# Kernel tuning notes

Measured on AMD Instinct MI355X. Metric: run time of the kernel, lower is better.

The kernel has to match this reference:

```python
import jax, jax.numpy as jnp
import numpy as np

B, T, TC, C, CC, H = 2, 2048, 512, 1024, 512, 16
D = C // H  # head dim = 64


def setup_inputs() -> dict:
    key = jax.random.key(0)
    ks = jax.random.split(key, 18)
    w = lambda k, i, o: (jax.random.normal(k, (i, o), jnp.float32) / np.sqrt(i).astype(np.float32))
    return {
        "x": jax.random.normal(ks[0], (B, T, C), jnp.float32),
        "cross_input": jax.random.normal(ks[1], (B, TC, CC), jnp.float32),
        "Wk": w(ks[2], C, C),  "bk": jnp.zeros((C,), jnp.float32),
        "Wq": w(ks[3], C, C),  "bq": jnp.zeros((C,), jnp.float32),
        "Wv": w(ks[4], C, C),  "bv": jnp.zeros((C,), jnp.float32),
        "Wck": w(ks[5], CC, C), "bck": jnp.zeros((C,), jnp.float32),
        "Wcq": w(ks[6], C, C),  "bcq": jnp.zeros((C,), jnp.float32),
        "Wcv": w(ks[7], CC, C), "bcv": jnp.zeros((C,), jnp.float32),
        "Wp": w(ks[8], C, C),   "bp": jnp.zeros((C,), jnp.float32),
    }


def _heads(t):
    # [B, L, C] -> [B, H, L, D]
    b, l, _ = t.shape
    return t.reshape(b, l, H, D).transpose(0, 2, 1, 3)


def reference(x, cross_input, Wk, bk, Wq, bq, Wv, bv, Wck, bck, Wcq, bcq, Wcv, bcv, Wp, bp):
    scale = np.float32(1.0 / np.sqrt(D))
    q = _heads(x @ Wq + bq)
    k = _heads(x @ Wk + bk)
    v = _heads(x @ Wv + bv)
    # causal self-attention with materialized scores (faithful to original)
    att = jnp.einsum("bhqd,bhkd->bhqk", q, k) * scale
    causal = jnp.tril(jnp.ones((T, T), bool))
    att = jnp.where(causal[None, None], att, -jnp.inf)
    y = jnp.einsum("bhqk,bhkd->bhqd", jax.nn.softmax(att, axis=-1), v)
    # cross-attention (no mask)
    qc = _heads(x @ Wcq + bcq)
    kc = _heads(cross_input @ Wck + bck)
    vc = _heads(cross_input @ Wcv + bcv)
    attc = jnp.einsum("bhqd,bhkd->bhqk", qc, kc) * scale
    y = y + jnp.einsum("bhqk,bhkd->bhqd", jax.nn.softmax(attc, axis=-1), vc)
    # merge heads + output projection (dropout prob = 0 -> identity)
    y = y.transpose(0, 2, 1, 3).reshape(x.shape[0], T, C)
    return y @ Wp + bp
```

## Files before the change

### kernel.cpp

```cpp
#include <hip/hip_runtime.h>
#include <hip/hip_bf16.h>
#include <type_traits>

typedef __bf16 bf16;
typedef __bf16 bf16x8 __attribute__((ext_vector_type(8)));
typedef float floatx4 __attribute__((ext_vector_type(4)));
typedef unsigned int uint32x4 __attribute__((ext_vector_type(4)));

#if __has_builtin(__builtin_amdgcn_exp2f)
#define EXP2(x) __builtin_amdgcn_exp2f(x)
#else
#define EXP2(x) exp2f(x)
#endif

__device__ __forceinline__ void glds16(const bf16* g, bf16* l) {
  __builtin_amdgcn_global_load_lds((const __attribute__((address_space(1))) void*)g,
                                   (__attribute__((address_space(3))) void*)l, 16, 0, 0);
}

__device__ __forceinline__ unsigned pack_bf16(float a, float b) {
  unsigned short ua = __builtin_bit_cast(unsigned short, (bf16)a);
  unsigned short ub = __builtin_bit_cast(unsigned short, (bf16)b);
  return (unsigned)ua | ((unsigned)ub << 16);
}

struct PrepArgs {
  const float* x; const float* xc;
  bf16* xbf; bf16* xcbf;
  const float* b4[4];
  const float* bc[2];
  float* bias4; float* biasc;
  const float* W[7];
  bf16* WT[7];
};

__global__ __launch_bounds__(256) void prep_kernel(PrepArgs a) {
  __shared__ bf16 tsh[32][33];
  const int bx = blockIdx.x, tid = threadIdx.x;
  if (bx < 4096) {
    int i = bx * 256 + tid;
    float4 f = ((const float4*)a.x)[i];
    bf16 t[4] = {(bf16)f.x, (bf16)f.y, (bf16)f.z, (bf16)f.w};
    *(uint2*)&a.xbf[(long)i * 4] = *(const uint2*)t;
  } else if (bx < 4608) {
    int i = (bx - 4096) * 256 + tid;
    float4 f = ((const float4*)a.xc)[i];
    bf16 t[4] = {(bf16)f.x, (bf16)f.y, (bf16)f.z, (bf16)f.w};
    *(uint2*)&a.xcbf[(long)i * 4] = *(const uint2*)t;
  } else if (bx < 4632) {
    int lb = bx - 4608;
    if (lb < 16) {
      int i = lb * 256 + tid;
      int sec = i >> 10;
      float v = a.b4[sec][i & 1023];
      if (sec == 0 || sec == 3) v *= 0.18033688f;
      a.bias4[i] = v;
    } else {
      int i = (lb - 16) * 256 + tid;
      a.biasc[i] = a.bc[i >> 10][i & 1023];
    }
  } else {
    int t = bx - 4632, w, R, bxw, byw;
    if (t < 5120) { w = t >> 10; R = 1024; int l = t & 1023; bxw = l & 31; byw = l >> 5; }
    else { int t2 = t - 5120; w = 5 + (t2 >> 9); R = 512; int l = t2 & 511; bxw = l & 31; byw = l >> 5; }
    const float* in = a.W[w];
    bf16* out = a.WT[w];
    const float sc = (w == 0 || w == 3) ? 0.18033688f : 1.0f;
    int tx = tid & 31, ty = tid >> 5;
    int c = bxw * 32 + tx;
#pragma unroll
    for (int i = 0; i < 4; i++) {
      int r = byw * 32 + ty + i * 8;
      tsh[ty + i * 8][tx] = (bf16)(in[(long)r * 1024 + c] * sc);
    }
    __syncthreads();
    int oc = byw * 32 + tx;
#pragma unroll
    for (int i = 0; i < 4; i++) {
      int orr = bxw * 32 + ty + i * 8;
      out[(long)orr * R + oc] = tsh[tx][ty + i * 8];
    }
  }
}

template <typename OutT>
__global__ __launch_bounds__(256, 4) void gemm128(const bf16* __restrict__ A,
                                                  const bf16* __restrict__ Bt,
                                                  const float* __restrict__ bias,
                                                  OutT* __restrict__ C,
                                                  int M, int N, int K, int ldc,
                                                  bf16* __restrict__ Vt,
                                                  int vcol0, int vcol1, int Lt, int tok_shift) {
  __shared__ alignas(16) bf16 As[128 * 32];
  __shared__ alignas(16) bf16 Bs[128 * 32];
  const int tid = threadIdx.x, wave = tid >> 6, lane = tid & 63;
  const int l16 = lane & 15, l4 = lane >> 4;
  const int wm = wave & 1, wn = wave >> 1;
  const int nwg = gridDim.x * gridDim.y;
  int lin = blockIdx.y * gridDim.x + blockIdx.x;
  lin = (lin & 7) * (nwg >> 3) + (lin >> 3);
  const int n0 = (lin % gridDim.x) * 128, m0 = (lin / gridDim.x) * 128;
  const int lrow = lane >> 2, lch = (lane & 3) * 8;

  floatx4 acc[4][4];
#pragma unroll
  for (int mt = 0; mt < 4; mt++)
#pragma unroll
    for (int nt = 0; nt < 4; nt++) acc[mt][nt] = (floatx4){0.f, 0.f, 0.f, 0.f};

  const bf16* Ag = A + (long)(m0 + wave * 32 + lrow) * K + lch;
  const bf16* Bg = Bt + (long)(n0 + wave * 32 + lrow) * K + lch;
  bf16* Al = &As[(wave * 32) * 32];
  bf16* Bl = &Bs[(wave * 32) * 32];

  for (int k0 = 0; k0 < K; k0 += 32) {
    __syncthreads();
    glds16(Ag + k0, Al);
    glds16(Ag + k0 + (long)16 * K, Al + 16 * 32);
    glds16(Bg + k0, Bl);
    glds16(Bg + k0 + (long)16 * K, Bl + 16 * 32);
    __syncthreads();
    bf16x8 a[4], b[4];
#pragma unroll
    for (int mt = 0; mt < 4; mt++) a[mt] = *(const bf16x8*)&As[(wm * 64 + mt * 16 + l16) * 32 + l4 * 8];
#pragma unroll
    for (int nt = 0; nt < 4; nt++) b[nt] = *(const bf16x8*)&Bs[(wn * 64 + nt * 16 + l16) * 32 + l4 * 8];
#pragma unroll
    for (int mt = 0; mt < 4; mt++)
#pragma unroll
      for (int nt = 0; nt < 4; nt++)
        acc[mt][nt] = __builtin_amdgcn_mfma_f32_16x16x32_bf16(a[mt], b[nt], acc[mt][nt], 0, 0, 0);
  }

  const bool vpath = (vcol0 >= 0) && (n0 >= vcol0) && (n0 < vcol1);
  if (!vpath) {
    const int coladj = (vcol0 >= 0 && n0 >= vcol1) ? (vcol1 - vcol0) : 0;
#pragma unroll
    for (int nt = 0; nt < 4; nt++) {
      int col = n0 + wn * 64 + nt * 16 + l16;
      float bv = bias[col];
#pragma unroll
      for (int mt = 0; mt < 4; mt++)
#pragma unroll
        for (int r = 0; r < 4; r++) {
          int row = m0 + wm * 64 + mt * 16 + l4 * 4 + r;
          float v = acc[mt][nt][r] + bv;
          if constexpr (std::is_same_v<OutT, float>) C[(long)row * ldc + col - coladj] = v;
          else                                       C[(long)row * ldc + col - coladj] = (bf16)v;
        }
    }
  } else {
#pragma unroll
    for (int nt = 0; nt < 4; nt++) {
      int col = n0 + wn * 64 + nt * 16 + l16;
      int c = col - vcol0, hh = c >> 6, dd = c & 63;
      float bv = bias[col];
#pragma unroll
      for (int mt = 0; mt < 4; mt++) {
        int t0 = m0 + wm * 64 + mt * 16 + l4 * 4;
        int bb = t0 >> tok_shift, t = t0 & ((1 << tok_shift) - 1);
        t = (t & ~31) | (((t >> 2) & 3) << 3) | (((t >> 4) & 1) << 2) | (t & 3);
        bf16 tmp[4];
#pragma unroll
        for (int r = 0; r < 4; r++) tmp[r] = (bf16)(acc[mt][nt][r] + bv);
        *(uint2*)&Vt[(((long)bb * 16 + hh) * 64 + dd) * Lt + t] = *(const uint2*)tmp;
      }
    }
  }
}

__global__ __launch_bounds__(256, 2) void attn_kernel(const bf16* __restrict__ QKQc,
                                                      const bf16* __restrict__ VtB,
                                                      const bf16* __restrict__ KcB,
                                                      const bf16* __restrict__ VctB,
                                                      bf16* __restrict__ Y) {
  __shared__ float Lbuf[4][4][16];
  __shared__ alignas(16) bf16 U2[4 * 64 * 40];
  __shared__ alignas(16) float Osave[256][20];
  __shared__ alignas(16) bf16 Vsl[4][2][2048];
  const int tid = threadIdx.x, w = tid >> 6, lane = tid & 63;
  const int l16 = lane & 15, l4 = lane >> 4;
  const int bh = blockIdx.x, h = bh & 15, b = bh >> 4;
  const int wk = w * 32;
  const float NEG = -1e30f;
  const int swv = (l4 ^ ((l16 >> 1) & 3)) * 8;

  for (int qi = 0; qi < 2; qi++) {
    const int qt = qi ? (int)blockIdx.y : 31 - (int)blockIdx.y;
    const int q0 = qt * 64;

    for (int phase = 0; phase < 2; phase++) {
      const bf16 *Qb, *Kb, *Vtb;
      int kstr, vtstr, nkt;
      if (phase == 0) {
        Qb = QKQc + (long)b * 2048 * 3072 + h * 64;
        Kb = Qb + 1024;                              kstr = 3072;
        Vtb = VtB + ((long)b * 16 + h) * 64 * 2048;  vtstr = 2048;
        nkt = (qt + 2) >> 1;
      } else {
        Qb = QKQc + (long)b * 2048 * 3072 + h * 64 + 2048;
        Kb = KcB + (long)b * 512 * 1024 + h * 64;    kstr = 1024;
        Vtb = VctB + ((long)b * 16 + h) * 64 * 512;  vtstr = 512;
        nkt = 4;
      }

      __syncthreads();

      bf16x8 qf[4][2];
#pragma unroll
      for (int qtt = 0; qtt < 4; qtt++) {
        const bf16* qp = Qb + (long)(q0 + qtt * 16 + l16) * 3072 + l4 * 8;
#pragma unroll
        for (int ds = 0; ds < 2; ds++) qf[qtt][ds] = *(const bf16x8*)(qp + ds * 32);
      }

      float l_i[4];
#pragma unroll
      for (int qtt = 0; qtt < 4; qtt++) l_i[qtt] = 0.f;
      floatx4 oacc[4][4];
#pragma unroll
      for (int mtd = 0; mtd < 4; mtd++)
#pragma unroll
        for (int qtt = 0; qtt < 4; qtt++) oacc[mtd][qtt] = (floatx4){0.f, 0.f, 0.f, 0.f};

      bf16x8 kreg[2][2];
#pragma unroll
      for (int mt = 0; mt < 2; mt++)
#pragma unroll
        for (int ds = 0; ds < 2; ds++)
          kreg[mt][ds] = *(const bf16x8*)(Kb + (long)(wk + mt * 16 + l16) * kstr + ds * 32 + l4 * 8);
#pragma unroll
      for (int i = 0; i < 4; i++) {
        int c = i * 64 + lane, r = c >> 2;
        int kc = ((c & 3) ^ ((r >> 1) & 3)) * 8;
        glds16(Vtb + (long)r * vtstr + wk + kc, &Vsl[w][0][i * 512]);
      }

      floatx4 sacc[2][4];
#pragma unroll
      for (int mt = 0; mt < 2; mt++)
#pragma unroll
        for (int qtt = 0; qtt < 4; qtt++) sacc[mt][qtt] = (floatx4){0.f, 0.f, 0.f, 0.f};
#pragma unroll
      for (int ds = 0; ds < 2; ds++)
#pragma unroll
        for (int mt = 0; mt < 2; mt++)
#pragma unroll
          for (int qtt = 0; qtt < 4; qtt++)
            sacc[mt][qtt] = __builtin_amdgcn_mfma_f32_16x16x32_bf16(kreg[mt][ds], qf[qtt][ds], sacc[mt][qtt], 0, 0, 0);

      for (int kt = 0; kt < nkt; kt++) {
        const int kbase = kt * 128 + wk;
        const bool more = (kt + 1 < nkt);

        if (more) {
          bf16* dst = &Vsl[w][(kt + 1) & 1][0];
          const int nb = kbase + 128;
#pragma unroll
          for (int i = 0; i < 4; i++) {
            int c = i * 64 + lane, r = c >> 2;
            int kc = ((c & 3) ^ ((r >> 1) & 3)) * 8;
            glds16(Vtb + (long)r * vtstr + nb + kc, dst + i * 512);
          }
        }

        if (phase == 0 && kt == nkt - 1) {
#pragma unroll
          for (int mt = 0; mt < 2; mt++) {
            int keyb = kbase + mt * 16 + l4 * 4;
#pragma unroll
            for (int qtt = 0; qtt < 4; qtt++) {
              int q = q0 + qtt * 16 + l16;
#pragma unroll
              for (int r = 0; r < 4; r++)
                if (keyb + r > q) sacc[mt][qtt][r] = NEG;
            }
          }
        }

        bf16x8 vc[4];
        {
          const bf16* sl = &Vsl[w][kt & 1][0];
          if (more) asm volatile("s_waitcnt vmcnt(4)" ::: "memory");
          else      asm volatile("s_waitcnt vmcnt(0)" ::: "memory");
#pragma unroll
          for (int mtd = 0; mtd < 4; mtd++)
            vc[mtd] = *(const bf16x8*)&sl[(mtd * 16 + l16) * 32 + swv];
        }

        if (more) {
          const int nb = kbase + 128;
#pragma unroll
          for (int mt = 0; mt < 2; mt++)
#pragma unroll
            for (int ds = 0; ds < 2; ds++)
              kreg[mt][ds] = *(const bf16x8*)(Kb + (long)(nb + mt * 16 + l16) * kstr + ds * 32 + l4 * 8);
        }

#pragma unroll
        for (int qtt = 0; qtt < 4; qtt++) {
          float p0 = EXP2(sacc[0][qtt][0]), p1 = EXP2(sacc[0][qtt][1]);
          float p2 = EXP2(sacc[0][qtt][2]), p3 = EXP2(sacc[0][qtt][3]);
          float p4 = EXP2(sacc[1][qtt][0]), p5 = EXP2(sacc[1][qtt][1]);
          float p6 = EXP2(sacc[1][qtt][2]), p7 = EXP2(sacc[1][qtt][3]);
          l_i[qtt] += ((p0 + p1) + (p2 + p3)) + ((p4 + p5) + (p6 + p7));
          uint32x4 pu = {pack_bf16(p0, p1), pack_bf16(p2, p3), pack_bf16(p4, p5), pack_bf16(p6, p7)};
          bf16x8 pf = __builtin_bit_cast(bf16x8, pu);
          __builtin_amdgcn_s_setprio(1);
#pragma unroll
          for (int mtd = 0; mtd < 4; mtd++)
            oacc[mtd][qtt] = __builtin_amdgcn_mfma_f32_16x16x32_bf16(vc[mtd], pf, oacc[mtd][qtt], 0, 0, 0);
          __builtin_amdgcn_s_setprio(0);
        }

        if (more) {
#pragma unroll
          for (int mt = 0; mt < 2; mt++)
#pragma unroll
            for (int qtt = 0; qtt < 4; qtt++) sacc[mt][qtt] = (floatx4){0.f, 0.f, 0.f, 0.f};
          __builtin_amdgcn_s_setprio(1);
#pragma unroll
          for (int ds = 0; ds < 2; ds++)
#pragma unroll
            for (int mt = 0; mt < 2; mt++)
#pragma unroll
              for (int qtt = 0; qtt < 4; qtt++)
                sacc[mt][qtt] = __builtin_amdgcn_mfma_f32_16x16x32_bf16(kreg[mt][ds], qf[qtt][ds], sacc[mt][qtt], 0, 0, 0);
          __builtin_amdgcn_s_setprio(0);
        }
      }

      float lsum[4];
#pragma unroll
      for (int qtt = 0; qtt < 4; qtt++) {
        float r = l_i[qtt];
        r += __shfl_xor(r, 16);
        r += __shfl_xor(r, 32);
        lsum[qtt] = r;
      }
      if (l4 == 0) {
#pragma unroll
        for (int qtt = 0; qtt < 4; qtt++) Lbuf[w][qtt][l16] = lsum[qtt];
      }
      float sum[16];
#pragma unroll
      for (int j = 0; j < 16; j++) sum[j] = 0.f;
      float denom = 0.f;
#pragma unroll
      for (int p = 0; p < 2; p++) {
        __syncthreads();
#pragma unroll
        for (int qtt = 0; qtt < 4; qtt++)
#pragma unroll
          for (int mm = 0; mm < 2; mm++) {
            int mtd = p * 2 + mm;
            uint2 u = {pack_bf16(oacc[mtd][qtt][0], oacc[mtd][qtt][1]),
                       pack_bf16(oacc[mtd][qtt][2], oacc[mtd][qtt][3])};
            *(uint2*)&U2[((w * 64) + qtt * 16 + l16) * 40 + mm * 16 + l4 * 4] = u;
          }
        __syncthreads();
        if (p == 0)
          denom = Lbuf[0][w][l16] + Lbuf[1][w][l16] + Lbuf[2][w][l16] + Lbuf[3][w][l16];
        if ((l4 >> 1) == p) {
#pragma unroll
          for (int s = 0; s < 4; s++) {
            bf16x8 c0 = *(const bf16x8*)&U2[((s * 64) + w * 16 + l16) * 40 + (l4 & 1) * 16];
            bf16x8 c1 = *(const bf16x8*)&U2[((s * 64) + w * 16 + l16) * 40 + (l4 & 1) * 16 + 8];
#pragma unroll
            for (int j = 0; j < 8; j++) { sum[j] += (float)c0[j]; sum[8 + j] += (float)c1[j]; }
          }
        }
      }
      float invd = 1.0f / denom;
      if (phase == 0) {
#pragma unroll
        for (int jj = 0; jj < 4; jj++) {
          float4 v = {sum[jj * 4] * invd, sum[jj * 4 + 1] * invd,
                      sum[jj * 4 + 2] * invd, sum[jj * 4 + 3] * invd};
          *(float4*)&Osave[tid][jj * 4] = v;
        }
      } else {
        long row = (long)b * 2048 + q0 + w * 16 + l16;
        bf16 out[16];
#pragma unroll
        for (int jj = 0; jj < 4; jj++) {
          float4 v = *(const float4*)&Osave[tid][jj * 4];
          out[jj * 4]     = (bf16)(v.x + sum[jj * 4] * invd);
          out[jj * 4 + 1] = (bf16)(v.y + sum[jj * 4 + 1] * invd);
          out[jj * 4 + 2] = (bf16)(v.z + sum[jj * 4 + 2] * invd);
          out[jj * 4 + 3] = (bf16)(v.w + sum[jj * 4 + 3] * invd);
        }
        *(bf16x8*)&Y[row * 1024 + h * 64 + l4 * 16] = *(const bf16x8*)&out[0];
        *(bf16x8*)&Y[row * 1024 + h * 64 + l4 * 16 + 8] = *(const bf16x8*)&out[8];
      }
    }
  }
}

extern "C" void kernel_launch(void* const* d_in, const int* in_sizes, int n_in,
                              void* d_out, int out_size, void* d_ws, size_t ws_size,
                              hipStream_t stream) {
  const float* x   = (const float*)d_in[0];
  const float* xc  = (const float*)d_in[1];
  const float* Wk  = (const float*)d_in[2];  const float* bk  = (const float*)d_in[3];
  const float* Wq  = (const float*)d_in[4];  const float* bq  = (const float*)d_in[5];
  const float* Wv  = (const float*)d_in[6];  const float* bv  = (const float*)d_in[7];
  const float* Wck = (const float*)d_in[8];  const float* bck = (const float*)d_in[9];
  const float* Wcq = (const float*)d_in[10]; const float* bcq = (const float*)d_in[11];
  const float* Wcv = (const float*)d_in[12]; const float* bcv = (const float*)d_in[13];
  const float* Wp  = (const float*)d_in[14]; const float* bp  = (const float*)d_in[15];

  char* ws = (char*)d_ws;
  const size_t MB = 1ull << 20;
  bf16*  WT_all = (bf16*)(ws + 0);
  bf16*  WC_all = (bf16*)(ws + 8 * MB);
  bf16*  WpT    = (bf16*)(ws + 10 * MB);
  bf16*  xbf    = (bf16*)(ws + 12 * MB);
  bf16*  Yb     = xbf;
  bf16*  xcbf   = (bf16*)(ws + 20 * MB);
  float* bias4  = (float*)(ws + 21 * MB);
  float* biasc  = (float*)(ws + 21 * MB + 65536);
  bf16*  QKQc   = (bf16*)(ws + 22 * MB);
  bf16*  VtB    = (bf16*)(ws + 46 * MB);
  bf16*  KcB    = (bf16*)(ws + 54 * MB);
  bf16*  VctB   = (bf16*)(ws + 56 * MB);

  PrepArgs pa;
  pa.x = x; pa.xc = xc; pa.xbf = xbf; pa.xcbf = xcbf;
  pa.b4[0] = bq; pa.b4[1] = bk; pa.b4[2] = bv; pa.b4[3] = bcq;
  pa.bc[0] = bck; pa.bc[1] = bcv;
  pa.bias4 = bias4; pa.biasc = biasc;
  pa.W[0] = Wq;  pa.WT[0] = WT_all + 0ll * 1024 * 1024;
  pa.W[1] = Wk;  pa.WT[1] = WT_all + 1ll * 1024 * 1024;
  pa.W[2] = Wv;  pa.WT[2] = WT_all + 2ll * 1024 * 1024;
  pa.W[3] = Wcq; pa.WT[3] = WT_all + 3ll * 1024 * 1024;
  pa.W[4] = Wp;  pa.WT[4] = WpT;
  pa.W[5] = Wck; pa.WT[5] = WC_all + 0ll * 1024 * 512;
  pa.W[6] = Wcv; pa.WT[6] = WC_all + 1ll * 1024 * 512;
  prep_kernel<<<10776, 256, 0, stream>>>(pa);

  gemm128<bf16><<<dim3(32, 32), 256, 0, stream>>>(xbf, WT_all, bias4, QKQc,
                                                  4096, 4096, 1024, 3072,
                                                  VtB, 2048, 3072, 2048, 11);
  gemm128<bf16><<<dim3(16, 8), 256, 0, stream>>>(xcbf, WC_all, biasc, KcB,
                                                 1024, 2048, 512, 1024,
                                                 VctB, 1024, 2048, 512, 9);

  attn_kernel<<<dim3(32, 16), 256, 0, stream>>>(QKQc, VtB, KcB, VctB, Yb);

  gemm128<float><<<dim3(8, 32), 256, 0, stream>>>(Yb, WpT, bp, (float*)d_out,
                                                  4096, 1024, 1024, 1024,
                                                  nullptr, -1, -1, 0, 0);
}
```

Measured before the change: 245.8 us.

## Give each attention block one query tile and shrink LDS footprint

Result: no change. 243.1 us (-1.1%).

```diff
diff --git a/kernel.cpp b/kernel.cpp
--- a/kernel.cpp
+++ b/kernel.cpp
@@ -176,223 +176,214 @@
                                                       bf16* __restrict__ Y) {
   __shared__ float Lbuf[4][4][16];
   __shared__ alignas(16) bf16 U2[4 * 64 * 40];
-  __shared__ alignas(16) float Osave[256][20];
-  __shared__ alignas(16) bf16 Vsl[4][2][2048];
+  __shared__ alignas(16) bf16 Osave[256][24];
+  __shared__ alignas(16) bf16 Vsl[4][2048];
   const int tid = threadIdx.x, w = tid >> 6, lane = tid & 63;
   const int l16 = lane & 15, l4 = lane >> 4;
   const int bh = blockIdx.x, h = bh & 15, b = bh >> 4;
+  const int qt = 31 - (int)blockIdx.y;
+  const int q0 = qt * 64;
   const int wk = w * 32;
   const float NEG = -1e30f;
   const int swv = (l4 ^ ((l16 >> 1) & 3)) * 8;
 
-  for (int qi = 0; qi < 2; qi++) {
-    const int qt = qi ? (int)blockIdx.y : 31 - (int)blockIdx.y;
-    const int q0 = qt * 64;
-
-    for (int phase = 0; phase < 2; phase++) {
-      const bf16 *Qb, *Kb, *Vtb;
-      int kstr, vtstr, nkt;
-      if (phase == 0) {
-        Qb = QKQc + (long)b * 2048 * 3072 + h * 64;
-        Kb = Qb + 1024;                              kstr = 3072;
-        Vtb = VtB + ((long)b * 16 + h) * 64 * 2048;  vtstr = 2048;
-        nkt = (qt + 2) >> 1;
-      } else {
-        Qb = QKQc + (long)b * 2048 * 3072 + h * 64 + 2048;
-        Kb = KcB + (long)b * 512 * 1024 + h * 64;    kstr = 1024;
-        Vtb = VctB + ((long)b * 16 + h) * 64 * 512;  vtstr = 512;
-        nkt = 4;
-      }
-
-      __syncthreads();
-
-      bf16x8 qf[4][2];
-#pragma unroll
-      for (int qtt = 0; qtt < 4; qtt++) {
-        const bf16* qp = Qb + (long)(q0 + qtt * 16 + l16) * 3072 + l4 * 8;
-#pragma unroll
-        for (int ds = 0; ds < 2; ds++) qf[qtt][ds] = *(const bf16x8*)(qp + ds * 32);
-      }
-
-      float l_i[4];
-#pragma unroll
-      for (int qtt = 0; qtt < 4; qtt++) l_i[qtt] = 0.f;
-      floatx4 oacc[4][4];
-#pragma unroll
-      for (int mtd = 0; mtd < 4; mtd++)
-#pragma unroll
-        for (int qtt = 0; qtt < 4; qtt++) oacc[mtd][qtt] = (floatx4){0.f, 0.f, 0.f, 0.f};
-
-      bf16x8 kreg[2][2];
+  for (int phase = 0; phase < 2; phase++) {
+    const bf16 *Qb, *Kb, *Vtb;
+    int kstr, vtstr, nkt;
+    if (phase == 0) {
+      Qb = QKQc + (long)b * 2048 * 3072 + h * 64;
+      Kb = Qb + 1024;                              kstr = 3072;
+      Vtb = VtB + ((long)b * 16 + h) * 64 * 2048;  vtstr = 2048;
+      nkt = (qt + 2) >> 1;
+    } else {
+      Qb = QKQc + (long)b * 2048 * 3072 + h * 64 + 2048;
+      Kb = KcB + (long)b * 512 * 1024 + h * 64;    kstr = 1024;
+      Vtb = VctB + ((long)b * 16 + h) * 64 * 512;  vtstr = 512;
+      nkt = 4;
+    }
+
+    __syncthreads();
+
+    bf16x8 qf[4][2];
+#pragma unroll
+    for (int qtt = 0; qtt < 4; qtt++) {
+      const bf16* qp = Qb + (long)(q0 + qtt * 16 + l16) * 3072 + l4 * 8;
+#pragma unroll
+      for (int ds = 0; ds < 2; ds++) qf[qtt][ds] = *(const bf16x8*)(qp + ds * 32);
+    }
+
+    float l_i[4];
+#pragma unroll
+    for (int qtt = 0; qtt < 4; qtt++) l_i[qtt] = 0.f;
+    floatx4 oacc[4][4];
+#pragma unroll
+    for (int mtd = 0; mtd < 4; mtd++)
+#pragma unroll
+      for (int qtt = 0; qtt < 4; qtt++) oacc[mtd][qtt] = (floatx4){0.f, 0.f, 0.f, 0.f};
+
+    bf16x8 kreg[2][2];
+#pragma unroll
+    for (int mt = 0; mt < 2; mt++)
+#pragma unroll
+      for (int ds = 0; ds < 2; ds++)
+        kreg[mt][ds] = *(const bf16x8*)(Kb + (long)(wk + mt * 16 + l16) * kstr + ds * 32 + l4 * 8);
+#pragma unroll
+    for (int i = 0; i < 4; i++) {
+      int c = i * 64 + lane, r = c >> 2;
+      int kc = ((c & 3) ^ ((r >> 1) & 3)) * 8;
+      glds16(Vtb + (long)r * vtstr + wk + kc, &Vsl[w][i * 512]);
+    }
+
+    floatx4 sacc[2][4];
+#pragma unroll
+    for (int mt = 0; mt < 2; mt++)
+#pragma unroll
+      for (int qtt = 0; qtt < 4; qtt++) sacc[mt][qtt] = (floatx4){0.f, 0.f, 0.f, 0.f};
+#pragma unroll
+    for (int ds = 0; ds < 2; ds++)
 #pragma unroll
       for (int mt = 0; mt < 2; mt++)
 #pragma unroll
-        for (int ds = 0; ds < 2; ds++)
-          kreg[mt][ds] = *(const bf16x8*)(Kb + (long)(wk + mt * 16 + l16) * kstr + ds * 32 + l4 * 8);
-#pragma unroll
-      for (int i = 0; i < 4; i++) {
-        int c = i * 64 + lane, r = c >> 2;
-        int kc = ((c & 3) ^ ((r >> 1) & 3)) * 8;
-        glds16(Vtb + (long)r * vtstr + wk + kc, &Vsl[w][0][i * 512]);
-      }
-
-      floatx4 sacc[2][4];
-#pragma unroll
-      for (int mt = 0; mt < 2; mt++)
-#pragma unroll
-        for (int qtt = 0; qtt < 4; qtt++) sacc[mt][qtt] = (floatx4){0.f, 0.f, 0.f, 0.f};
-#pragma unroll
-      for (int ds = 0; ds < 2; ds++)
-#pragma unroll
-        for (int mt = 0; mt < 2; mt++)
-#pragma unroll
-          for (int qtt = 0; qtt < 4; qtt++)
-            sacc[mt][qtt] = __builtin_amdgcn_mfma_f32_16x16x32_bf16(kreg[mt][ds], qf[qtt][ds], sacc[mt][qtt], 0, 0, 0);
-
-      for (int kt = 0; kt < nkt; kt++) {
-        const int kbase = kt * 128 + wk;
-        const bool more = (kt + 1 < nkt);
-
-        if (more) {
-          bf16* dst = &Vsl[w][(kt + 1) & 1][0];
-          const int nb = kbase + 128;
-#pragma unroll
-          for (int i = 0; i < 4; i++) {
-            int c = i * 64 + lane, r = c >> 2;
-            int kc = ((c & 3) ^ ((r >> 1) & 3)) * 8;
-            glds16(Vtb + (long)r * vtstr + nb + kc, dst + i * 512);
+        for (int qtt = 0; qtt < 4; qtt++)
+          sacc[mt][qtt] = __builtin_amdgcn_mfma_f32_16x16x32_bf16(kreg[mt][ds], qf[qtt][ds], sacc[mt][qtt], 0, 0, 0);
+
+    for (int kt = 0; kt < nkt; kt++) {
+      const int kbase = kt * 128 + wk;
+      const bool more = (kt + 1 < nkt);
+
+      if (phase == 0 && kt == nkt - 1) {
+#pragma unroll
+        for (int mt = 0; mt < 2; mt++) {
+          int keyb = kbase + mt * 16 + l4 * 4;
+#pragma unroll
+          for (int qtt = 0; qtt < 4; qtt++) {
+            int q = q0 + qtt * 16 + l16;
+#pragma unroll
+            for (int r = 0; r < 4; r++)
+              if (keyb + r > q) sacc[mt][qtt][r] = NEG;
           }
         }
-
-        if (phase == 0 && kt == nkt - 1) {
-#pragma unroll
-          for (int mt = 0; mt < 2; mt++) {
-            int keyb = kbase + mt * 16 + l4 * 4;
-#pragma unroll
-            for (int qtt = 0; qtt < 4; qtt++) {
-              int q = q0 + qtt * 16 + l16;
-#pragma unroll
-              for (int r = 0; r < 4; r++)
-                if (keyb + r > q) sacc[mt][qtt][r] = NEG;
-            }
-          }
+      }
+
+      asm volatile("s_waitcnt vmcnt(0)" ::: "memory");
+      bf16x8 vc[4];
+      {
+        const bf16* sl = &Vsl[w][0];
+#pragma unroll
+        for (int mtd = 0; mtd < 4; mtd++)
+          vc[mtd] = *(const bf16x8*)&sl[(mtd * 16 + l16) * 32 + swv];
+      }
+      asm volatile("s_waitcnt lgkmcnt(0)" ::: "memory");
+
+      if (more) {
+        const int nb = kbase + 128;
+#pragma unroll
+        for (int mt = 0; mt < 2; mt++)
+#pragma unroll
+          for (int ds = 0; ds < 2; ds++)
+            kreg[mt][ds] = *(const bf16x8*)(Kb + (long)(nb + mt * 16 + l16) * kstr + ds * 32 + l4 * 8);
+        bf16* dst = &Vsl[w][0];
+#pragma unroll
+        for (int i = 0; i < 4; i++) {
+          int c = i * 64 + lane, r = c >> 2;
+          int kc = ((c & 3) ^ ((r >> 1) & 3)) * 8;
+          glds16(Vtb + (long)r * vtstr + nb + kc, dst + i * 512);
         }
-
-        bf16x8 vc[4];
-        {
-          const bf16* sl = &Vsl[w][kt & 1][0];
-          if (more) asm volatile("s_waitcnt vmcnt(4)" ::: "memory");
-          else      asm volatile("s_waitcnt vmcnt(0)" ::: "memory");
-#pragma unroll
-          for (int mtd = 0; mtd < 4; mtd++)
-            vc[mtd] = *(const bf16x8*)&sl[(mtd * 16 + l16) * 32 + swv];
+      }
+
+#pragma unroll
+      for (int qtt = 0; qtt < 4; qtt++) {
+        float p0 = EXP2(sacc[0][qtt][0]), p1 = EXP2(sacc[0][qtt][1]);
+        float p2 = EXP2(sacc[0][qtt][2]), p3 = EXP2(sacc[0][qtt][3]);
+        float p4 = EXP2(sacc[1][qtt][0]), p5 = EXP2(sacc[1][qtt][1]);
+        float p6 = EXP2(sacc[1][qtt][2]), p7 = EXP2(sacc[1][qtt][3]);
+        l_i[qtt] += ((p0 + p1) + (p2 + p3)) + ((p4 + p5) + (p6 + p7));
+        uint32x4 pu = {pack_bf16(p0, p1), pack_bf16(p2, p3), pack_bf16(p4, p5), pack_bf16(p6, p7)};
+        bf16x8 pf = __builtin_bit_cast(bf16x8, pu);
+        __builtin_amdgcn_s_setprio(1);
+#pragma unroll
+        for (int mtd = 0; mtd < 4; mtd++)
+          oacc[mtd][qtt] = __builtin_amdgcn_mfma_f32_16x16x32_bf16(vc[mtd], pf, oacc[mtd][qtt], 0, 0, 0);
+        __builtin_amdgcn_s_setprio(0);
+      }
+
+      if (more) {
+#pragma unroll
+        for (int mt = 0; mt < 2; mt++)
+#pragma unroll
+          for (int qtt = 0; qtt < 4; qtt++) sacc[mt][qtt] = (floatx4){0.f, 0.f, 0.f, 0.f};
+        __builtin_amdgcn_s_setprio(1);
+#pragma unroll
+        for (int ds = 0; ds < 2; ds++)
+#pragma unroll
+          for (int mt = 0; mt < 2; mt++)
+#pragma unroll
+            for (int qtt = 0; qtt < 4; qtt++)
+              sacc[mt][qtt] = __builtin_amdgcn_mfma_f32_16x16x32_bf16(kreg[mt][ds], qf[qtt][ds], sacc[mt][qtt], 0, 0, 0);
+        __builtin_amdgcn_s_setprio(0);
+      }
+    }
+
+    float lsum[4];
+#pragma unroll
+    for (int qtt = 0; qtt < 4; qtt++) {
+      float r = l_i[qtt];
+      r += __shfl_xor(r, 16);
+      r += __shfl_xor(r, 32);
+      lsum[qtt] = r;
+    }
+    if (l4 == 0) {
+#pragma unroll
+      for (int qtt = 0; qtt < 4; qtt++) Lbuf[w][qtt][l16] = lsum[qtt];
+    }
+    float sum[16];
+#pragma unroll
+    for (int j = 0; j < 16; j++) sum[j] = 0.f;
+    float denom = 0.f;
+#pragma unroll
+    for (int p = 0; p < 2; p++) {
+      __syncthreads();
+#pragma unroll
+      for (int qtt = 0; qtt < 4; qtt++)
+#pragma unroll
+        for (int mm = 0; mm < 2; mm++) {
+          int mtd = p * 2 + mm;
+          uint2 u = {pack_bf16(oacc[mtd][qtt][0], oacc[mtd][qtt][1]),
+                     pack_bf16(oacc[mtd][qtt][2], oacc[mtd][qtt][3])};
+          *(uint2*)&U2[((w * 64) + qtt * 16 + l16) * 40 + mm * 16 + l4 * 4] = u;
         }
-
-        if (more) {
-          const int nb = kbase + 128;
-#pragma unroll
-          for (int mt = 0; mt < 2; mt++)
-#pragma unroll
-            for (int ds = 0; ds < 2; ds++)
-              kreg[mt][ds] = *(const bf16x8*)(Kb + (long)(nb + mt * 16 + l16) * kstr + ds * 32 + l4 * 8);
+      __syncthreads();
+      if (p == 0)
+        denom = Lbuf[0][w][l16] + Lbuf[1][w][l16] + Lbuf[2][w][l16] + Lbuf[3][w][l16];
+      if ((l4 >> 1) == p) {
+#pragma unroll
+        for (int s = 0; s < 4; s++) {
+          bf16x8 c0 = *(const bf16x8*)&U2[((s * 64) + w * 16 + l16) * 40 + (l4 & 1) * 16];
+          bf16x8 c1 = *(const bf16x8*)&U2[((s * 64) + w * 16 + l16) * 40 + (l4 & 1) * 16 + 8];
+#pragma unroll
+          for (int j = 0; j < 8; j++) { sum[j] += (float)c0[j]; sum[8 + j] += (float)c1[j]; }
         }
-
-#pragma unroll
-        for (int qtt = 0; qtt < 4; qtt++) {
-          float p0 = EXP2(sacc[0][qtt][0]), p1 = EXP2(sacc[0][qtt][1]);
-          float p2 = EXP2(sacc[0][qtt][2]), p3 = EXP2(sacc[0][qtt][3]);
-          float p4 = EXP2(sacc[1][qtt][0]), p5 = EXP2(sacc[1][qtt][1]);
-          float p6 = EXP2(sacc[1][qtt][2]), p7 = EXP2(sacc[1][qtt][3]);
-          l_i[qtt] += ((p0 + p1) + (p2 + p3)) + ((p4 + p5) + (p6 + p7));
-          uint32x4 pu = {pack_bf16(p0, p1), pack_bf16(p2, p3), pack_bf16(p4, p5), pack_bf16(p6, p7)};
-          bf16x8 pf = __builtin_bit_cast(bf16x8, pu);
-          __builtin_amdgcn_s_setprio(1);
-#pragma unroll
-          for (int mtd = 0; mtd < 4; mtd++)
-            oacc[mtd][qtt] = __builtin_amdgcn_mfma_f32_16x16x32_bf16(vc[mtd], pf, oacc[mtd][qtt], 0, 0, 0);
-          __builtin_amdgcn_s_setprio(0);
-        }
-
-        if (more) {
-#pragma unroll
-          for (int mt = 0; mt < 2; mt++)
-#pragma unroll
-            for (int qtt = 0; qtt < 4; qtt++) sacc[mt][qtt] = (floatx4){0.f, 0.f, 0.f, 0.f};
-          __builtin_amdgcn_s_setprio(1);
-#pragma unroll
-          for (int ds = 0; ds < 2; ds++)
-#pragma unroll
-            for (int mt = 0; mt < 2; mt++)
-#pragma unroll
-              for (int qtt = 0; qtt < 4; qtt++)
-                sacc[mt][qtt] = __builtin_amdgcn_mfma_f32_16x16x32_bf16(kreg[mt][ds], qf[qtt][ds], sacc[mt][qtt], 0, 0, 0);
-          __builtin_amdgcn_s_setprio(0);
-        }
-      }
-
-      float lsum[4];
-#pragma unroll
-      for (int qtt = 0; qtt < 4; qtt++) {
-        float r = l_i[qtt];
-        r += __shfl_xor(r, 16);
-        r += __shfl_xor(r, 32);
-        lsum[qtt] = r;
-      }
-      if (l4 == 0) {
-#pragma unroll
-        for (int qtt = 0; qtt < 4; qtt++) Lbuf[w][qtt][l16] = lsum[qtt];
-      }
-      float sum[16];
-#pragma unroll
-      for (int j = 0; j < 16; j++) sum[j] = 0.f;
-      float denom = 0.f;
-#pragma unroll
-      for (int p = 0; p < 2; p++) {
-        __syncthreads();
-#pragma unroll
-        for (int qtt = 0; qtt < 4; qtt++)
-#pragma unroll
-          for (int mm = 0; mm < 2; mm++) {
-            int mtd = p * 2 + mm;
-            uint2 u = {pack_bf16(oacc[mtd][qtt][0], oacc[mtd][qtt][1]),
-                       pack_bf16(oacc[mtd][qtt][2], oacc[mtd][qtt][3])};
-            *(uint2*)&U2[((w * 64) + qtt * 16 + l16) * 40 + mm * 16 + l4 * 4] = u;
-          }
-        __syncthreads();
-        if (p == 0)
-          denom = Lbuf[0][w][l16] + Lbuf[1][w][l16] + Lbuf[2][w][l16] + Lbuf[3][w][l16];
-        if ((l4 >> 1) == p) {
-#pragma unroll
-          for (int s = 0; s < 4; s++) {
-            bf16x8 c0 = *(const bf16x8*)&U2[((s * 64) + w * 16 + l16) * 40 + (l4 & 1) * 16];
-            bf16x8 c1 = *(const bf16x8*)&U2[((s * 64) + w * 16 + l16) * 40 + (l4 & 1) * 16 + 8];
-#pragma unroll
-            for (int j = 0; j < 8; j++) { sum[j] += (float)c0[j]; sum[8 + j] += (float)c1[j]; }
-          }
-        }
-      }
-      float invd = 1.0f / denom;
-      if (phase == 0) {
-#pragma unroll
-        for (int jj = 0; jj < 4; jj++) {
-          float4 v = {sum[jj * 4] * invd, sum[jj * 4 + 1] * invd,
-                      sum[jj * 4 + 2] * invd, sum[jj * 4 + 3] * invd};
-          *(float4*)&Osave[tid][jj * 4] = v;
-        }
-      } else {
-        long row = (long)b * 2048 + q0 + w * 16 + l16;
-        bf16 out[16];
-#pragma unroll
-        for (int jj = 0; jj < 4; jj++) {
-          float4 v = *(const float4*)&Osave[tid][jj * 4];
-          out[jj * 4]     = (bf16)(v.x + sum[jj * 4] * invd);
-          out[jj * 4 + 1] = (bf16)(v.y + sum[jj * 4 + 1] * invd);
-          out[jj * 4 + 2] = (bf16)(v.z + sum[jj * 4 + 2] * invd);
-          out[jj * 4 + 3] = (bf16)(v.w + sum[jj * 4 + 3] * invd);
-        }
-        *(bf16x8*)&Y[row * 1024 + h * 64 + l4 * 16] = *(const bf16x8*)&out[0];
-        *(bf16x8*)&Y[row * 1024 + h * 64 + l4 * 16 + 8] = *(const bf16x8*)&out[8];
-      }
+      }
+    }
+    float invd = 1.0f / denom;
+    if (phase == 0) {
+      bf16 so[16];
+#pragma unroll
+      for (int j = 0; j < 16; j++) so[j] = (bf16)(sum[j] * invd);
+      *(bf16x8*)&Osave[tid][0] = *(const bf16x8*)&so[0];
+      *(bf16x8*)&Osave[tid][8] = *(const bf16x8*)&so[8];
+    } else {
+      long row = (long)b * 2048 + q0 + w * 16 + l16;
+      bf16x8 s0 = *(const bf16x8*)&Osave[tid][0];
+      bf16x8 s1 = *(const bf16x8*)&Osave[tid][8];
+      bf16 out[16];
+#pragma unroll
+      for (int j = 0; j < 8; j++) {
+        out[j]     = (bf16)((float)s0[j] + sum[j] * invd);
+        out[8 + j] = (bf16)((float)s1[j] + sum[8 + j] * invd);
+      }
+      *(bf16x8*)&Y[row * 1024 + h * 64 + l4 * 16] = *(const bf16x8*)&out[0];
+      *(bf16x8*)&Y[row * 1024 + h * 64 + l4 * 16 + 8] = *(const bf16x8*)&out[8];
     }
   }
 }
@@ -446,7 +437,7 @@
                                                  1024, 2048, 512, 1024,
                                                  VctB, 1024, 2048, 512, 9);
 
-  attn_kernel<<<dim3(32, 16), 256, 0, stream>>>(QKQc, VtB, KcB, VctB, Yb);
+  attn_kernel<<<dim3(32, 32), 256, 0, stream>>>(QKQc, VtB, KcB, VctB, Yb);
 
   gemm128<float><<<dim3(8, 32), 256, 0, stream>>>(Yb, WpT, bp, (float*)d_out,
                                                   4096, 1024, 1024, 1024,
```
